# Optimization experiments

Measured on AMD Instinct MI355X. Metric: run time of the kernel, lower is better.

Reference implementation:

```python
import jax, jax.numpy as jnp
import numpy as np

N = 100000   # support / query points
H = 32       # neighbors per query
C = 64       # channels
K = 15       # kernel points (sum(shell_sizes)=1+14)
RADIUS = 1.0
SIGMA = 0.3
INF = 1.0e6  # shadow-point coordinate


def setup_inputs() -> dict:
    key = jax.random.key(0)
    k0, k1, k2, k3, k4, k5 = jax.random.split(key, 6)
    s_pts = jax.random.uniform(k0, (N, 3), dtype=jnp.float32) * (2.0 * RADIUS)
    q_pts = jax.random.uniform(k1, (N, 3), dtype=jnp.float32) * (2.0 * RADIUS)
    s_feats = jax.random.normal(k2, (N, C), dtype=jnp.float32)
    neighb_inds = jax.random.randint(k3, (N, H), 0, N)
    # kaiming_uniform_(a=sqrt(5)) on (K, C): bound = 1/sqrt(fan_in) = 1/sqrt(C)
    bound = 1.0 / np.sqrt(C)
    weights = jax.random.uniform(k4, (K, C), dtype=jnp.float32, minval=-bound, maxval=bound)
    # kernel point dispositions within the ball of RADIUS; center point fixed at origin
    kernel_points = jax.random.normal(k5, (K, 3), dtype=jnp.float32) * (0.5 * RADIUS)
    kernel_points = kernel_points.at[0].set(0.0)
    return {
        "q_pts": q_pts,
        "s_pts": s_pts,
        "s_feats": s_feats,
        "neighb_inds": neighb_inds,
        "weights": weights,
        "kernel_points": kernel_points,
    }


def reference(q_pts, s_pts, s_feats, neighb_inds, weights, kernel_points):
    M = q_pts.shape[0]
    Cc = s_feats.shape[1]
    # pad with shadow point (far away) / zero feature row so out-of-range idx == N
    s_pts_pad = jnp.concatenate([s_pts, jnp.full((1, 3), INF, s_pts.dtype)], axis=0)
    s_feats_pad = jnp.concatenate([s_feats, jnp.zeros((1, Cc), s_feats.dtype)], axis=0)

    neighbor_feats = s_feats_pad[neighb_inds]                 # [M, H, C]
    neighbors = s_pts_pad[neighb_inds] - q_pts[:, None, :]    # [M, H, 3]

    # squared distance to each kernel point, nearest-kernel assignment
    diffs = neighbors[:, :, None, :] - kernel_points[None, None, :, :]  # [M, H, K, 3]
    sq_dists = jnp.sum(diffs * diffs, axis=-1)                # [M, H, K]
    nn_sq_dists = jnp.min(sq_dists, axis=2)                   # [M, H]
    neighbors_1nn = jnp.argmin(sq_dists, axis=2)              # [M, H]

    # linear influence
    influence = jnp.clip(1.0 - jnp.sqrt(nn_sq_dists) / SIGMA, 0.0)  # [M, H]

    # depthwise (Cmid=0): gather per-kernel-point weights, modulate, sum over neighbors
    neighbors_weights = weights[neighbors_1nn] * influence[..., None]  # [M, H, C]
    output_feats = jnp.sum(neighbor_feats * neighbors_weights, axis=1)  # [M, C]
    return output_feats
```

## Files before the change

kernel.cpp:

```cpp
#include <hip/hip_runtime.h>

#define H 32
#define C 64
#define K 15
#define SIGMA 0.3f
#define WAVES 4

__global__ __launch_bounds__(256) void kpconv_kernel(
    const float* __restrict__ q_pts,
    const float* __restrict__ s_pts,
    const float* __restrict__ s_feats,
    const int*   __restrict__ inds,
    const float* __restrict__ weights,
    const float* __restrict__ kpts,
    float*       __restrict__ out,
    int N)
{
    __shared__ float2 list[WAVES][2][32];

    const int tid  = threadIdx.x;
    const int wave = tid >> 6;
    const int lane = tid & 63;
    const int half = lane >> 5;
    const int hl   = lane & 31;
    const int mBase = blockIdx.x * (WAVES * 2) + wave * 2;
    const int m = mBase + half;

    float kp[K * 3];
    #pragma unroll
    for (int i = 0; i < K * 3; ++i) kp[i] = kpts[i];

    float infl   = 0.0f;
    int   packed = 0;
    if (m < N) {
        const int idx = inds[m * H + hl];
        if (idx >= 0 && idx < N) {
            const float qx = q_pts[m * 3 + 0];
            const float qy = q_pts[m * 3 + 1];
            const float qz = q_pts[m * 3 + 2];
            const float nx = s_pts[idx * 3 + 0] - qx;
            const float ny = s_pts[idx * 3 + 1] - qy;
            const float nz = s_pts[idx * 3 + 2] - qz;
            float best = 1e30f;
            int   kbest = 0;
            #pragma unroll
            for (int k = 0; k < K; ++k) {
                const float dx = nx - kp[k * 3 + 0];
                const float dy = ny - kp[k * 3 + 1];
                const float dz = nz - kp[k * 3 + 2];
                const float d2 = dx * dx + dy * dy + dz * dz;
                if (d2 < best) { best = d2; kbest = k; }
            }
            infl = 1.0f - sqrtf(best) / SIGMA;
            if (infl < 0.0f) infl = 0.0f;
            packed = idx | (kbest << 20);
        }
    }

    const unsigned long long ball = __ballot(infl > 0.0f);
    const unsigned int maskH = half ? (unsigned int)(ball >> 32)
                                    : (unsigned int)(ball & 0xFFFFFFFFu);
    const int rank = __popc(maskH & ((1u << hl) - 1u));
    if (infl > 0.0f)
        list[wave][half][rank] = make_float2(__int_as_float(packed), infl);
    const int cnt = __popc(maskH);

    float2 acc = make_float2(0.0f, 0.0f);
    const float2* wrows = (const float2*)weights;
    for (int i = 0; i < cnt; i += 2) {
        const float4 pf = *(const float4*)&list[wave][half][i];
        const int   p0   = __float_as_int(pf.x);
        const float f0   = pf.y;
        const bool  has1 = (i + 1) < cnt;
        const int   p1   = has1 ? __float_as_int(pf.z) : 0;
        const float f1   = has1 ? pf.w : 0.0f;
        const float2 a0 = ((const float2*)(s_feats + (size_t)(p0 & 0xFFFFF) * C))[hl];
        const float2 w0 = wrows[(p0 >> 20) * (C / 2) + hl];
        const float2 a1 = ((const float2*)(s_feats + (size_t)(p1 & 0xFFFFF) * C))[hl];
        const float2 w1 = wrows[(p1 >> 20) * (C / 2) + hl];
        acc.x += a0.x * w0.x * f0;
        acc.y += a0.y * w0.y * f0;
        acc.x += a1.x * w1.x * f1;
        acc.y += a1.y * w1.y * f1;
    }

    if (m < N)
        *(float2*)(out + (size_t)m * C + hl * 2) = acc;
}

extern "C" void kernel_launch(void* const* d_in, const int* in_sizes, int n_in,
                              void* d_out, int out_size, void* d_ws, size_t ws_size,
                              hipStream_t stream) {
    const float* q_pts   = (const float*)d_in[0];
    const float* s_pts   = (const float*)d_in[1];
    const float* s_feats = (const float*)d_in[2];
    const int*   inds    = (const int*)d_in[3];
    const float* weights = (const float*)d_in[4];
    const float* kpts    = (const float*)d_in[5];
    float* out = (float*)d_out;

    const int N = in_sizes[0] / 3;
    const int blocks = (N + WAVES * 2 - 1) / (WAVES * 2);
    kpconv_kernel<<<blocks, 256, 0, stream>>>(q_pts, s_pts, s_feats, inds,
                                              weights, kpts, out, N);
}
```

Before: 35.86 us.

## Make waves persistent and prefetch next pair's indices and points

```diff
diff --git a/kernel.cpp b/kernel.cpp
--- a/kernel.cpp
+++ b/kernel.cpp
@@ -5,6 +5,7 @@
 #define K 15
 #define SIGMA 0.3f
 #define WAVES 4
+#define PAIRS_PER_WAVE 7
 
 __global__ __launch_bounds__(256) void kpconv_kernel(
     const float* __restrict__ q_pts,
@@ -23,26 +24,42 @@
     const int lane = tid & 63;
     const int half = lane >> 5;
     const int hl   = lane & 31;
-    const int mBase = blockIdx.x * (WAVES * 2) + wave * 2;
-    const int m = mBase + half;
 
     float kp[K * 3];
     #pragma unroll
     for (int i = 0; i < K * 3; ++i) kp[i] = kpts[i];
 
-    float infl   = 0.0f;
-    int   packed = 0;
-    if (m < N) {
-        const int idx = inds[m * H + hl];
-        if (idx >= 0 && idx < N) {
-            const float qx = q_pts[m * 3 + 0];
-            const float qy = q_pts[m * 3 + 1];
-            const float qz = q_pts[m * 3 + 2];
-            const float nx = s_pts[idx * 3 + 0] - qx;
-            const float ny = s_pts[idx * 3 + 1] - qy;
-            const float nz = s_pts[idx * 3 + 2] - qz;
-            float best = 1e30f;
-            int   kbest = 0;
+    const int nPairs = (N + 1) >> 1;
+    const int waveId = blockIdx.x * WAVES + wave;
+    const int stride = gridDim.x * WAVES;
+
+    int pair = waveId;
+    if (pair >= nPairs) return;
+
+    int  mC   = pair * 2 + half;
+    int  idxC = (mC < N) ? inds[mC * H + hl] : -1;
+    bool okC  = (idxC >= 0) && (idxC < N);
+    {
+        const int ia = okC ? idxC : 0;
+        (void)ia;
+    }
+    const int ia0 = okC ? idxC : 0;
+    float sxC = s_pts[ia0 * 3 + 0], syC = s_pts[ia0 * 3 + 1], szC = s_pts[ia0 * 3 + 2];
+    float qxC = 0.f, qyC = 0.f, qzC = 0.f;
+    if (mC < N) { qxC = q_pts[mC * 3 + 0]; qyC = q_pts[mC * 3 + 1]; qzC = q_pts[mC * 3 + 2]; }
+
+    while (true) {
+        const int  pairN   = pair + stride;
+        const bool hasNext = pairN < nPairs;
+        const int  mN      = pairN * 2 + half;
+
+        int idxN = -1;
+        if (hasNext && mN < N) idxN = inds[mN * H + hl];
+
+        float infl = 0.0f; int packed = 0;
+        if (okC && (mC < N)) {
+            const float nx = sxC - qxC, ny = syC - qyC, nz = szC - qzC;
+            float best = 1e30f; int kbest = 0;
             #pragma unroll
             for (int k = 0; k < K; ++k) {
                 const float dx = nx - kp[k * 3 + 0];
@@ -53,39 +70,52 @@
             }
             infl = 1.0f - sqrtf(best) / SIGMA;
             if (infl < 0.0f) infl = 0.0f;
-            packed = idx | (kbest << 20);
+            packed = idxC | (kbest << 20);
         }
+
+        const unsigned long long ball = __ballot(infl > 0.0f);
+        const unsigned int maskH = half ? (unsigned int)(ball >> 32)
+                                        : (unsigned int)(ball & 0xFFFFFFFFu);
+        const int rank = __popc(maskH & ((1u << hl) - 1u));
+        if (infl > 0.0f)
+            list[wave][half][rank] = make_float2(__int_as_float(packed), infl);
+        const int cnt = __popc(maskH);
+
+        float sxN = 0.f, syN = 0.f, szN = 0.f, qxN = 0.f, qyN = 0.f, qzN = 0.f;
+        bool  okN = false;
+        if (hasNext) {
+            okN = (idxN >= 0) && (idxN < N);
+            const int ib = okN ? idxN : 0;
+            sxN = s_pts[ib * 3 + 0]; syN = s_pts[ib * 3 + 1]; szN = s_pts[ib * 3 + 2];
+            if (mN < N) { qxN = q_pts[mN * 3 + 0]; qyN = q_pts[mN * 3 + 1]; qzN = q_pts[mN * 3 + 2]; }
+        }
+
+        float2 acc = make_float2(0.0f, 0.0f);
+        const float2* wrows = (const float2*)weights;
+        for (int i = 0; i < cnt; i += 2) {
+            const float4 pf = *(const float4*)&list[wave][half][i];
+            const int   p0   = __float_as_int(pf.x);
+            const float f0   = pf.y;
+            const bool  has1 = (i + 1) < cnt;
+            const int   p1   = has1 ? __float_as_int(pf.z) : 0;
+            const float f1   = has1 ? pf.w : 0.0f;
+            const float2 a0 = ((const float2*)(s_feats + (size_t)(p0 & 0xFFFFF) * C))[hl];
+            const float2 w0 = wrows[(p0 >> 20) * (C / 2) + hl];
+            const float2 a1 = ((const float2*)(s_feats + (size_t)(p1 & 0xFFFFF) * C))[hl];
+            const float2 w1 = wrows[(p1 >> 20) * (C / 2) + hl];
+            acc.x += a0.x * w0.x * f0;
+            acc.y += a0.y * w0.y * f0;
+            acc.x += a1.x * w1.x * f1;
+            acc.y += a1.y * w1.y * f1;
+        }
+        if (mC < N)
+            *(float2*)(out + (size_t)mC * C + hl * 2) = acc;
+
+        if (!hasNext) break;
+        pair = pairN; mC = mN; idxC = idxN; okC = okN;
+        sxC = sxN; syC = syN; szC = szN;
+        qxC = qxN; qyC = qyN; qzC = qzN;
     }
-
-    const unsigned long long ball = __ballot(infl > 0.0f);
-    const unsigned int maskH = half ? (unsigned int)(ball >> 32)
-                                    : (unsigned int)(ball & 0xFFFFFFFFu);
-    const int rank = __popc(maskH & ((1u << hl) - 1u));
-    if (infl > 0.0f)
-        list[wave][half][rank] = make_float2(__int_as_float(packed), infl);
-    const int cnt = __popc(maskH);
-
-    float2 acc = make_float2(0.0f, 0.0f);
-    const float2* wrows = (const float2*)weights;
-    for (int i = 0; i < cnt; i += 2) {
-        const float4 pf = *(const float4*)&list[wave][half][i];
-        const int   p0   = __float_as_int(pf.x);
-        const float f0   = pf.y;
-        const bool  has1 = (i + 1) < cnt;
-        const int   p1   = has1 ? __float_as_int(pf.z) : 0;
-        const float f1   = has1 ? pf.w : 0.0f;
-        const float2 a0 = ((const float2*)(s_feats + (size_t)(p0 & 0xFFFFF) * C))[hl];
-        const float2 w0 = wrows[(p0 >> 20) * (C / 2) + hl];
-        const float2 a1 = ((const float2*)(s_feats + (size_t)(p1 & 0xFFFFF) * C))[hl];
-        const float2 w1 = wrows[(p1 >> 20) * (C / 2) + hl];
-        acc.x += a0.x * w0.x * f0;
-        acc.y += a0.y * w0.y * f0;
-        acc.x += a1.x * w1.x * f1;
-        acc.y += a1.y * w1.y * f1;
-    }
-
-    if (m < N)
-        *(float2*)(out + (size_t)m * C + hl * 2) = acc;
 }
 
 extern "C" void kernel_launch(void* const* d_in, const int* in_sizes, int n_in,
@@ -100,7 +130,9 @@
     float* out = (float*)d_out;
 
     const int N = in_sizes[0] / 3;
-    const int blocks = (N + WAVES * 2 - 1) / (WAVES * 2);
+    const int nPairs = (N + 1) / 2;
+    int blocks = (nPairs + WAVES * PAIRS_PER_WAVE - 1) / (WAVES * PAIRS_PER_WAVE);
+    if (blocks < 1) blocks = 1;
     kpconv_kernel<<<blocks, 256, 0, stream>>>(q_pts, s_pts, s_feats, inds,
                                               weights, kpts, out, N);
 }
```

Result: slower. 46.11 us (+28.6%).

## Process four queries per wave with float4 feature gathers in accumulation

Applied to the files above, without the earlier changes.

```diff
diff --git a/kernel.cpp b/kernel.cpp
--- a/kernel.cpp
+++ b/kernel.cpp
@@ -5,6 +5,7 @@
 #define K 15
 #define SIGMA 0.3f
 #define WAVES 4
+#define QPW 4
 
 __global__ __launch_bounds__(256) void kpconv_kernel(
     const float* __restrict__ q_pts,
@@ -16,76 +17,92 @@
     float*       __restrict__ out,
     int N)
 {
-    __shared__ float2 list[WAVES][2][32];
+    __shared__ float2 list[WAVES][QPW][34];
 
     const int tid  = threadIdx.x;
     const int wave = tid >> 6;
     const int lane = tid & 63;
     const int half = lane >> 5;
     const int hl   = lane & 31;
-    const int mBase = blockIdx.x * (WAVES * 2) + wave * 2;
-    const int m = mBase + half;
 
     float kp[K * 3];
     #pragma unroll
     for (int i = 0; i < K * 3; ++i) kp[i] = kpts[i];
 
-    float infl   = 0.0f;
-    int   packed = 0;
-    if (m < N) {
-        const int idx = inds[m * H + hl];
-        if (idx >= 0 && idx < N) {
-            const float qx = q_pts[m * 3 + 0];
-            const float qy = q_pts[m * 3 + 1];
-            const float qz = q_pts[m * 3 + 2];
-            const float nx = s_pts[idx * 3 + 0] - qx;
-            const float ny = s_pts[idx * 3 + 1] - qy;
-            const float nz = s_pts[idx * 3 + 2] - qz;
-            float best = 1e30f;
-            int   kbest = 0;
-            #pragma unroll
-            for (int k = 0; k < K; ++k) {
-                const float dx = nx - kp[k * 3 + 0];
-                const float dy = ny - kp[k * 3 + 1];
-                const float dz = nz - kp[k * 3 + 2];
-                const float d2 = dx * dx + dy * dy + dz * dz;
-                if (d2 < best) { best = d2; kbest = k; }
+    const int qBase = (blockIdx.x * WAVES + wave) * QPW;
+
+    int c0 = 0, c1 = 0, c2 = 0, c3 = 0;
+
+    #pragma unroll
+    for (int p = 0; p < 2; ++p) {
+        const int m = qBase + p * 2 + half;
+        float infl = 0.0f;
+        int   packed = 0;
+        if (m < N) {
+            const int idx = inds[m * H + hl];
+            if (idx >= 0 && idx < N) {
+                const float qx = q_pts[m * 3 + 0];
+                const float qy = q_pts[m * 3 + 1];
+                const float qz = q_pts[m * 3 + 2];
+                const float nx = s_pts[idx * 3 + 0] - qx;
+                const float ny = s_pts[idx * 3 + 1] - qy;
+                const float nz = s_pts[idx * 3 + 2] - qz;
+                float best = 1e30f;
+                int   kbest = 0;
+                #pragma unroll
+                for (int k = 0; k < K; ++k) {
+                    const float dx = nx - kp[k * 3 + 0];
+                    const float dy = ny - kp[k * 3 + 1];
+                    const float dz = nz - kp[k * 3 + 2];
+                    const float d2 = dx * dx + dy * dy + dz * dz;
+                    if (d2 < best) { best = d2; kbest = k; }
+                }
+                infl = 1.0f - __builtin_amdgcn_sqrtf(best) * (1.0f / SIGMA);
+                if (infl < 0.0f) infl = 0.0f;
+                packed = idx | (kbest << 20);
             }
-            infl = 1.0f - sqrtf(best) / SIGMA;
-            if (infl < 0.0f) infl = 0.0f;
-            packed = idx | (kbest << 20);
+        }
+        const unsigned long long ball = __ballot(infl > 0.0f);
+        const unsigned int lo = (unsigned int)(ball & 0xFFFFFFFFu);
+        const unsigned int hi = (unsigned int)(ball >> 32);
+        const unsigned int maskH = half ? hi : lo;
+        const int rank = __popc(maskH & ((1u << hl) - 1u));
+        if (infl > 0.0f)
+            list[wave][p * 2 + half][rank] = make_float2(__int_as_float(packed), infl);
+        if (p == 0) { c0 = __popc(lo); c1 = __popc(hi); }
+        else        { c2 = __popc(lo); c3 = __popc(hi); }
+    }
+
+    const int q  = lane >> 4;
+    const int ql = lane & 15;
+    const int cq = (q < 2) ? (q == 0 ? c0 : c1) : (q == 2 ? c2 : c3);
+    int maxc = c0 > c1 ? c0 : c1;
+    if (c2 > maxc) maxc = c2;
+    if (c3 > maxc) maxc = c3;
+
+    float4 acc = make_float4(0.0f, 0.0f, 0.0f, 0.0f);
+    for (int i = 0; i < maxc; i += 2) {
+        if (i < cq) {
+            const float4 pf = *(const float4*)&list[wave][q][i];
+            const int   p0   = __float_as_int(pf.x);
+            const float f0   = pf.y;
+            const bool  has1 = (i + 1) < cq;
+            const int   p1   = has1 ? __float_as_int(pf.z) : 0;
+            const float f1   = has1 ? pf.w : 0.0f;
+            const float4 a0 = *(const float4*)(s_feats + (size_t)(p0 & 0xFFFFF) * C + ql * 4);
+            const float4 w0 = *(const float4*)(weights + (p0 >> 20) * C + ql * 4);
+            const float4 a1 = *(const float4*)(s_feats + (size_t)(p1 & 0xFFFFF) * C + ql * 4);
+            const float4 w1 = *(const float4*)(weights + (p1 >> 20) * C + ql * 4);
+            acc.x += a0.x * w0.x * f0;  acc.y += a0.y * w0.y * f0;
+            acc.z += a0.z * w0.z * f0;  acc.w += a0.w * w0.w * f0;
+            acc.x += a1.x * w1.x * f1;  acc.y += a1.y * w1.y * f1;
+            acc.z += a1.z * w1.z * f1;  acc.w += a1.w * w1.w * f1;
         }
     }
 
-    const unsigned long long ball = __ballot(infl > 0.0f);
-    const unsigned int maskH = half ? (unsigned int)(ball >> 32)
-                                    : (unsigned int)(ball & 0xFFFFFFFFu);
-    const int rank = __popc(maskH & ((1u << hl) - 1u));
-    if (infl > 0.0f)
-        list[wave][half][rank] = make_float2(__int_as_float(packed), infl);
-    const int cnt = __popc(maskH);
-
-    float2 acc = make_float2(0.0f, 0.0f);
-    const float2* wrows = (const float2*)weights;
-    for (int i = 0; i < cnt; i += 2) {
-        const float4 pf = *(const float4*)&list[wave][half][i];
-        const int   p0   = __float_as_int(pf.x);
-        const float f0   = pf.y;
-        const bool  has1 = (i + 1) < cnt;
-        const int   p1   = has1 ? __float_as_int(pf.z) : 0;
-        const float f1   = has1 ? pf.w : 0.0f;
-        const float2 a0 = ((const float2*)(s_feats + (size_t)(p0 & 0xFFFFF) * C))[hl];
-        const float2 w0 = wrows[(p0 >> 20) * (C / 2) + hl];
-        const float2 a1 = ((const float2*)(s_feats + (size_t)(p1 & 0xFFFFF) * C))[hl];
-        const float2 w1 = wrows[(p1 >> 20) * (C / 2) + hl];
-        acc.x += a0.x * w0.x * f0;
-        acc.y += a0.y * w0.y * f0;
-        acc.x += a1.x * w1.x * f1;
-        acc.y += a1.y * w1.y * f1;
-    }
-
-    if (m < N)
-        *(float2*)(out + (size_t)m * C + hl * 2) = acc;
+    const int mq = qBase + q;
+    if (mq < N)
+        *(float4*)(out + (size_t)mq * C + ql * 4) = acc;
 }
 
 extern "C" void kernel_launch(void* const* d_in, const int* in_sizes, int n_in,
@@ -100,7 +117,8 @@
     float* out = (float*)d_out;
 
     const int N = in_sizes[0] / 3;
-    const int blocks = (N + WAVES * 2 - 1) / (WAVES * 2);
+    const int qpb = WAVES * QPW;
+    const int blocks = (N + qpb - 1) / qpb;
     kpconv_kernel<<<blocks, 256, 0, stream>>>(q_pts, s_pts, s_feats, inds,
                                               weights, kpts, out, N);
 }
```

Result: faster. 33.36 us (-7.0%).
